# Optimization experiments

Hardware: AMD Instinct MI355X
Metric: run time of the kernel (lower is better)

Reference implementation:

```python
import jax, jax.numpy as jnp
import numpy as np

LOOKBACK = 8
EPS = 1e-6
HID = 32
MV_DIM = 11  # 1 scalar + 4 vector + 6 bivector
# default bivector planes (i, j)
BIV_I = jnp.array([0, 0, 0, 1, 1, 2])
BIV_J = jnp.array([1, 2, 3, 2, 3, 3])


def phi(x):
    # LeakyReLU(x, 0.01) + 1.0
    return jnp.where(x >= 0, x, 0.01 * x) + 1.0


def setup_inputs() -> dict:
    key = jax.random.key(0)
    ks = jax.random.split(key, 10)
    B, L = 8, 16384
    return {
        "x": jax.random.normal(ks[0], (B, L, 4), dtype=jnp.float32),
        "scalar_bias": jax.random.normal(ks[1], (1,), dtype=jnp.float32) * 0.1,
        "vector_scale": 1.0 + jax.random.normal(ks[2], (4,), dtype=jnp.float32) * 0.1,
        "vector_bias": jax.random.normal(ks[3], (4,), dtype=jnp.float32) * 0.1,
        "bivector_weight": 1.0 + jax.random.normal(ks[4], (6,), dtype=jnp.float32) * 0.1,
        "W_Q": jax.random.normal(ks[5], (MV_DIM, HID), dtype=jnp.float32) * 0.3,
        "W_K": jax.random.normal(ks[6], (MV_DIM, HID), dtype=jnp.float32) * 0.3,
        "W_V": jax.random.normal(ks[7], (MV_DIM, HID), dtype=jnp.float32) * 0.3,
        "w_head": jax.random.normal(ks[8], (HID,), dtype=jnp.float32) * 0.18,
        "b_head": jax.random.normal(ks[9], (), dtype=jnp.float32) * 0.1,
    }


def ga_embed(x, scalar_bias, vector_scale, vector_bias, bivector_weight):
    B, L, _ = x.shape
    scalar = jnp.broadcast_to(1.0 + scalar_bias, (B, L, 1))  # [B,L,1]
    vec = x * vector_scale + vector_bias                      # [B,L,4]
    biv = bivector_weight * (x[..., BIV_I] - x[..., BIV_J])   # [B,L,6]
    return jnp.concatenate([scalar, vec, biv], axis=-1)       # [B,L,11]


def reference(x, scalar_bias, vector_scale, vector_bias, bivector_weight,
              W_Q, W_K, W_V, w_head, b_head):
    M = ga_embed(x, scalar_bias, vector_scale, vector_bias, bivector_weight)
    B, L, _ = M.shape
    Q = phi(M @ W_Q)  # [B,L,H]
    K = phi(M @ W_K)
    V = M @ W_V
    T = L - LOOKBACK
    # sliding windows: for output step t (t = LOOKBACK..L-1) window covers [t-Lb, t)
    win_idx = jnp.arange(T)[:, None] + jnp.arange(LOOKBACK)[None, :]  # [T,Lb]
    Kw = K[:, win_idx]  # [B,T,Lb,H]
    Vw = V[:, win_idx]  # [B,T,Lb,H]
    q = Q[:, LOOKBACK:, :]  # [B,T,H]
    # scores_l = q_t . k_l ; num = sum_l scores_l v_l ; den = sum_l scores_l
    # (identical math to q . (sum_l k_l v_l^T) and q . sum_l k_l)
    scores = jnp.einsum('bth,btlh->btl', q, Kw)               # [B,T,Lb]
    num = jnp.einsum('btl,btlg->btg', scores, Vw)             # [B,T,H]
    den = jnp.sum(scores, axis=-1, keepdims=True) + EPS
    contexts = num / den                                      # [B,T,H]
    weights = scores / (jnp.sum(scores, axis=-1, keepdims=True) + EPS)
    predictions = contexts @ w_head + b_head                  # [B,T]
    return predictions, weights
```

## Files before the change

### kernel.cpp

```cpp
#include <hip/hip_runtime.h>

#define LOOKBACK 8
#define HID 32
#define TB 256
#define NPOS (TB + LOOKBACK)
#define KST 36
#define EPS 1e-6f

#define WS_AQ  0
#define WS_CQ  128
#define WS_AK  160
#define WS_CK  288
#define WS_AVW 320
#define WS_CVW 324
#define WS_N   336

__device__ __forceinline__ float phi1(float z) {
    return (z >= 0.0f ? z : 0.01f * z) + 1.0f;
}

__global__ __launch_bounds__(TB) void ga_fused(
    const float* __restrict__ x,
    const float* __restrict__ sbp,
    const float* __restrict__ vsp,
    const float* __restrict__ vbp,
    const float* __restrict__ bwp,
    const float* __restrict__ WQ,
    const float* __restrict__ WK,
    const float* __restrict__ WV,
    const float* __restrict__ wh,
    const float* __restrict__ bhp,
    float* __restrict__ out,
    int B, int L)
{
    const int T   = L - LOOKBACK;
    const int bb  = blockIdx.y;
    const int t0  = blockIdx.x * TB;
    const int tid = threadIdx.x;

    __shared__ float sP[WS_N];
    __shared__ float sK[NPOS * KST];
    __shared__ float sVW[NPOS];

    const int t = t0 + tid;
    const bool valid = (t < T);
    const float4 xq = *reinterpret_cast<const float4*>(
        x + ((size_t)bb * L + (valid ? t + LOOKBACK : 0)) * 4);

    if (tid < 96) {
        const int h   = tid & 31;
        const int mat = tid >> 5;
        const float* W = (mat == 0) ? WQ : (mat == 1) ? WK : WV;
        float w[11];
#pragma unroll
        for (int j = 0; j < 11; ++j) w[j] = W[j * HID + h];

        const float b0 = bwp[0], b1 = bwp[1], b2 = bwp[2];
        const float b3 = bwp[3], b4 = bwp[4], b5 = bwp[5];
        const float v0 = vsp[0], v1 = vsp[1], v2 = vsp[2], v3 = vsp[3];
        const float u0 = vbp[0], u1 = vbp[1], u2 = vbp[2], u3 = vbp[3];
        const float s0 = 1.0f + sbp[0];

        const float a0 = v0*w[1] + b0*w[5] + b1*w[6] + b2*w[7];
        const float a1 = v1*w[2] - b0*w[5] + b3*w[8] + b4*w[9];
        const float a2 = v2*w[3] - b1*w[6] - b3*w[8] + b5*w[10];
        const float a3 = v3*w[4] - b2*w[7] - b4*w[9] - b5*w[10];
        const float c  = s0*w[0] + u0*w[1] + u1*w[2] + u2*w[3] + u3*w[4];

        if (mat == 0) {
            sP[WS_AQ + 0*HID + h] = a0; sP[WS_AQ + 1*HID + h] = a1;
            sP[WS_AQ + 2*HID + h] = a2; sP[WS_AQ + 3*HID + h] = a3;
            sP[WS_CQ + h] = c;
        } else if (mat == 1) {
            sP[WS_AK + 0*HID + h] = a0; sP[WS_AK + 1*HID + h] = a1;
            sP[WS_AK + 2*HID + h] = a2; sP[WS_AK + 3*HID + h] = a3;
            sP[WS_CK + h] = c;
        } else {
            const float ww = wh[h];
            float r[5] = { a0*ww, a1*ww, a2*ww, a3*ww, c*ww };
#pragma unroll
            for (int off = 16; off > 0; off >>= 1) {
#pragma unroll
                for (int i = 0; i < 5; ++i) r[i] += __shfl_down(r[i], off, 32);
            }
            if (h == 0) {
                sP[WS_AVW + 0] = r[0]; sP[WS_AVW + 1] = r[1];
                sP[WS_AVW + 2] = r[2]; sP[WS_AVW + 3] = r[3];
                sP[WS_CVW]     = r[4];
            }
        }
    }
    __syncthreads();

    const float avw0 = sP[WS_AVW + 0], avw1 = sP[WS_AVW + 1];
    const float avw2 = sP[WS_AVW + 2], avw3 = sP[WS_AVW + 3];
    const float cvw  = sP[WS_CVW];

    const int npos = min(NPOS, L - t0);
    for (int pos = tid; pos < npos; pos += TB) {
        const float4 xv = *reinterpret_cast<const float4*>(
            x + ((size_t)bb * L + (t0 + pos)) * 4);

        sVW[pos] = cvw + xv.x*avw0 + xv.y*avw1 + xv.z*avw2 + xv.w*avw3;

#pragma unroll
        for (int g = 0; g < 8; ++g) {
            float4 a = *reinterpret_cast<const float4*>(&sP[WS_CK + g*4]);
#pragma unroll
            for (int d = 0; d < 4; ++d) {
                const float xd = (d == 0) ? xv.x : (d == 1) ? xv.y
                               : (d == 2) ? xv.z : xv.w;
                const float4 ad = *reinterpret_cast<const float4*>(
                    &sP[WS_AK + d*HID + g*4]);
                a.x += xd*ad.x; a.y += xd*ad.y; a.z += xd*ad.z; a.w += xd*ad.w;
            }
            a.x = phi1(a.x); a.y = phi1(a.y); a.z = phi1(a.z); a.w = phi1(a.w);
            *reinterpret_cast<float4*>(&sK[pos * KST + g * 4]) = a;
        }
    }
    __syncthreads();

    if (!valid) return;

    float q[HID];
#pragma unroll
    for (int g = 0; g < 8; ++g) {
        float4 z = *reinterpret_cast<const float4*>(&sP[WS_CQ + g*4]);
#pragma unroll
        for (int d = 0; d < 4; ++d) {
            const float xd = (d == 0) ? xq.x : (d == 1) ? xq.y
                           : (d == 2) ? xq.z : xq.w;
            const float4 ad = *reinterpret_cast<const float4*>(
                &sP[WS_AQ + d*HID + g*4]);
            z.x += xd*ad.x; z.y += xd*ad.y; z.z += xd*ad.z; z.w += xd*ad.w;
        }
        q[g*4+0] = phi1(z.x); q[g*4+1] = phi1(z.y);
        q[g*4+2] = phi1(z.z); q[g*4+3] = phi1(z.w);
    }

    float sc[LOOKBACK];
#pragma unroll
    for (int l = 0; l < LOOKBACK; ++l) sc[l] = 0.0f;

#pragma unroll
    for (int g = 0; g < 8; ++g) {
        const float qx = q[g*4+0], qy = q[g*4+1], qz = q[g*4+2], qw = q[g*4+3];
#pragma unroll
        for (int l = 0; l < LOOKBACK; ++l) {
            const float4 kg = *reinterpret_cast<const float4*>(
                &sK[(tid + l) * KST + g * 4]);
            sc[l] += qx*kg.x + qy*kg.y + qz*kg.z + qw*kg.w;
        }
    }

    float ssum = 0.0f, p = 0.0f;
#pragma unroll
    for (int l = 0; l < LOOKBACK; ++l) {
        ssum += sc[l];
        p    += sc[l] * sVW[tid + l];
    }
    const float inv = 1.0f / (ssum + EPS);

    out[(size_t)bb * T + t] = p * inv + bhp[0];

    float* wout = out + (size_t)B * T + ((size_t)bb * T + t) * LOOKBACK;
    *reinterpret_cast<float4*>(wout) =
        make_float4(sc[0]*inv, sc[1]*inv, sc[2]*inv, sc[3]*inv);
    *reinterpret_cast<float4*>(wout + 4) =
        make_float4(sc[4]*inv, sc[5]*inv, sc[6]*inv, sc[7]*inv);
}

extern "C" void kernel_launch(void* const* d_in, const int* in_sizes, int n_in,
                              void* d_out, int out_size, void* d_ws, size_t ws_size,
                              hipStream_t stream) {
    const float* x  = (const float*)d_in[0];
    const float* sb = (const float*)d_in[1];
    const float* vs = (const float*)d_in[2];
    const float* vb = (const float*)d_in[3];
    const float* bw = (const float*)d_in[4];
    const float* WQ = (const float*)d_in[5];
    const float* WK = (const float*)d_in[6];
    const float* WV = (const float*)d_in[7];
    const float* wh = (const float*)d_in[8];
    const float* bh = (const float*)d_in[9];
    float* out = (float*)d_out;

    const long long bl = (long long)in_sizes[0] / 4;
    const long long bt = (long long)out_size / (1 + LOOKBACK);
    const int B = (int)((bl - bt) / LOOKBACK);
    const int L = (int)(bl / B);
    const int T = L - LOOKBACK;

    dim3 grid((T + TB - 1) / TB, B);
    ga_fused<<<grid, TB, 0, stream>>>(x, sb, vs, vb, bw, WQ, WK, WV, wh, bh,
                                      out, B, L);
}
```

Baseline: 12.75 us.

## Compute two outputs per thread with group-major padded K layout in LDS

Halves the block to 128 threads, and each thread now handles two consecutive time steps, so the 9 K rows it loads serve both outputs' scores. K in shared memory moves from a row-major 36-float stride to a group-major layout with padding every 8 rows, meant to cut LDS bank conflicts on float4 reads. K and VW staging is unrolled to a fixed three rows per thread. The intent is fewer LDS reads per output and fewer block launches, at the cost of more registers per thread and a smaller block.

```diff
diff --git a/kernel.cpp b/kernel.cpp
--- a/kernel.cpp
+++ b/kernel.cpp
@@ -2,9 +2,9 @@
 
 #define LOOKBACK 8
 #define HID 32
-#define TB 256
-#define NPOS (TB + LOOKBACK)
-#define KST 36
+#define TB 128
+#define TPB 256
+#define NR  (TPB + LOOKBACK)
 #define EPS 1e-6f
 
 #define WS_AQ  0
@@ -15,37 +15,44 @@
 #define WS_CVW 324
 #define WS_N   336
 
+#define GSZ 1188
+
 __device__ __forceinline__ float phi1(float z) {
     return (z >= 0.0f ? z : 0.01f * z) + 1.0f;
 }
+__device__ __forceinline__ float dot4(const float4 a, const float4 b) {
+    return a.x*b.x + a.y*b.y + a.z*b.z + a.w*b.w;
+}
 
 __global__ __launch_bounds__(TB) void ga_fused(
     const float* __restrict__ x,
-    const float* __restrict__ sbp,
-    const float* __restrict__ vsp,
-    const float* __restrict__ vbp,
-    const float* __restrict__ bwp,
-    const float* __restrict__ WQ,
-    const float* __restrict__ WK,
-    const float* __restrict__ WV,
-    const float* __restrict__ wh,
+    const float* __restrict__ sbp, const float* __restrict__ vsp,
+    const float* __restrict__ vbp, const float* __restrict__ bwp,
+    const float* __restrict__ WQ,  const float* __restrict__ WK,
+    const float* __restrict__ WV,  const float* __restrict__ wh,
     const float* __restrict__ bhp,
     float* __restrict__ out,
     int B, int L)
 {
     const int T   = L - LOOKBACK;
     const int bb  = blockIdx.y;
-    const int t0  = blockIdx.x * TB;
+    const int t0  = blockIdx.x * TPB;
     const int tid = threadIdx.x;
 
     __shared__ float sP[WS_N];
-    __shared__ float sK[NPOS * KST];
-    __shared__ float sVW[NPOS];
-
-    const int t = t0 + tid;
-    const bool valid = (t < T);
-    const float4 xq = *reinterpret_cast<const float4*>(
-        x + ((size_t)bb * L + (valid ? t + LOOKBACK : 0)) * 4);
+    __shared__ float sK[8 * GSZ];
+    __shared__ float sVW[NR];
+
+    const float* xb = x + (size_t)bb * L * 4;
+
+    const int tl = 2 * tid;
+    const int ta = t0 + tl;
+    const bool va = (ta < T);
+    const bool vb = (ta + 1 < T);
+    const float4 xqa = *reinterpret_cast<const float4*>(
+        xb + (size_t)(va ? ta + LOOKBACK : 0) * 4);
+    const float4 xqb = *reinterpret_cast<const float4*>(
+        xb + (size_t)(vb ? ta + 1 + LOOKBACK : 0) * 4);
 
     if (tid < 96) {
         const int h   = tid & 31;
@@ -92,82 +99,141 @@
     }
     __syncthreads();
 
-    const float avw0 = sP[WS_AVW + 0], avw1 = sP[WS_AVW + 1];
-    const float avw2 = sP[WS_AVW + 2], avw3 = sP[WS_AVW + 3];
-    const float cvw  = sP[WS_CVW];
-
-    const int npos = min(NPOS, L - t0);
-    for (int pos = tid; pos < npos; pos += TB) {
-        const float4 xv = *reinterpret_cast<const float4*>(
-            x + ((size_t)bb * L + (t0 + pos)) * 4);
-
-        sVW[pos] = cvw + xv.x*avw0 + xv.y*avw1 + xv.z*avw2 + xv.w*avw3;
-
-#pragma unroll
-        for (int g = 0; g < 8; ++g) {
-            float4 a = *reinterpret_cast<const float4*>(&sP[WS_CK + g*4]);
-#pragma unroll
-            for (int d = 0; d < 4; ++d) {
-                const float xd = (d == 0) ? xv.x : (d == 1) ? xv.y
-                               : (d == 2) ? xv.z : xv.w;
-                const float4 ad = *reinterpret_cast<const float4*>(
-                    &sP[WS_AK + d*HID + g*4]);
-                a.x += xd*ad.x; a.y += xd*ad.y; a.z += xd*ad.z; a.w += xd*ad.w;
-            }
-            a.x = phi1(a.x); a.y = phi1(a.y); a.z = phi1(a.z); a.w = phi1(a.w);
-            *reinterpret_cast<float4*>(&sK[pos * KST + g * 4]) = a;
+    const int npos = min(NR, L - t0);
+    const int r0 = tid, r1 = tid + TB;
+    const bool has2 = (tid + 2*TB < npos);
+    const int r2 = tid + 2*TB;
+
+    const float4 x0 = *reinterpret_cast<const float4*>(xb + (size_t)(t0 + r0) * 4);
+    const float4 x1 = *reinterpret_cast<const float4*>(xb + (size_t)(t0 + r1) * 4);
+    const float4 x2 = *reinterpret_cast<const float4*>(
+        xb + (size_t)(has2 ? t0 + r2 : t0) * 4);
+
+    {
+        const float avw0 = sP[WS_AVW + 0], avw1 = sP[WS_AVW + 1];
+        const float avw2 = sP[WS_AVW + 2], avw3 = sP[WS_AVW + 3];
+        const float cvw  = sP[WS_CVW];
+        sVW[r0] = cvw + x0.x*avw0 + x0.y*avw1 + x0.z*avw2 + x0.w*avw3;
+        sVW[r1] = cvw + x1.x*avw0 + x1.y*avw1 + x1.z*avw2 + x1.w*avw3;
+        if (has2)
+            sVW[r2] = cvw + x2.x*avw0 + x2.y*avw1 + x2.z*avw2 + x2.w*avw3;
+    }
+
+    const int o0 = r0*4 + (r0>>3)*4;
+    const int o1 = r1*4 + (r1>>3)*4;
+    const int o2 = r2*4 + (r2>>3)*4;
+
+#pragma unroll
+    for (int g = 0; g < 8; ++g) {
+        const float4 c  = *reinterpret_cast<const float4*>(&sP[WS_CK + g*4]);
+        const float4 a0 = *reinterpret_cast<const float4*>(&sP[WS_AK + 0*HID + g*4]);
+        const float4 a1 = *reinterpret_cast<const float4*>(&sP[WS_AK + 1*HID + g*4]);
+        const float4 a2 = *reinterpret_cast<const float4*>(&sP[WS_AK + 2*HID + g*4]);
+        const float4 a3 = *reinterpret_cast<const float4*>(&sP[WS_AK + 3*HID + g*4]);
+
+        float4 k;
+        k.x = c.x + x0.x*a0.x + x0.y*a1.x + x0.z*a2.x + x0.w*a3.x;
+        k.y = c.y + x0.x*a0.y + x0.y*a1.y + x0.z*a2.y + x0.w*a3.y;
+        k.z = c.z + x0.x*a0.z + x0.y*a1.z + x0.z*a2.z + x0.w*a3.z;
+        k.w = c.w + x0.x*a0.w + x0.y*a1.w + x0.z*a2.w + x0.w*a3.w;
+        k.x = phi1(k.x); k.y = phi1(k.y); k.z = phi1(k.z); k.w = phi1(k.w);
+        *reinterpret_cast<float4*>(&sK[g*GSZ + o0]) = k;
+
+        k.x = c.x + x1.x*a0.x + x1.y*a1.x + x1.z*a2.x + x1.w*a3.x;
+        k.y = c.y + x1.x*a0.y + x1.y*a1.y + x1.z*a2.y + x1.w*a3.y;
+        k.z = c.z + x1.x*a0.z + x1.y*a1.z + x1.z*a2.z + x1.w*a3.z;
+        k.w = c.w + x1.x*a0.w + x1.y*a1.w + x1.z*a2.w + x1.w*a3.w;
+        k.x = phi1(k.x); k.y = phi1(k.y); k.z = phi1(k.z); k.w = phi1(k.w);
+        *reinterpret_cast<float4*>(&sK[g*GSZ + o1]) = k;
+
+        if (has2) {
+            k.x = c.x + x2.x*a0.x + x2.y*a1.x + x2.z*a2.x + x2.w*a3.x;
+            k.y = c.y + x2.x*a0.y + x2.y*a1.y + x2.z*a2.y + x2.w*a3.y;
+            k.z = c.z + x2.x*a0.z + x2.y*a1.z + x2.z*a2.z + x2.w*a3.z;
+            k.w = c.w + x2.x*a0.w + x2.y*a1.w + x2.z*a2.w + x2.w*a3.w;
+            k.x = phi1(k.x); k.y = phi1(k.y); k.z = phi1(k.z); k.w = phi1(k.w);
+            *reinterpret_cast<float4*>(&sK[g*GSZ + o2]) = k;
         }
     }
     __syncthreads();
 
-    if (!valid) return;
-
-    float q[HID];
+    if (!va) return;
+
+    float scA[LOOKBACK], scB[LOOKBACK];
+#pragma unroll
+    for (int l = 0; l < LOOKBACK; ++l) { scA[l] = 0.0f; scB[l] = 0.0f; }
+
+    int ro[9];
+#pragma unroll
+    for (int j = 0; j < 9; ++j) {
+        const int r = tl + j;
+        ro[j] = r*4 + (r>>3)*4;
+    }
+
 #pragma unroll
     for (int g = 0; g < 8; ++g) {
-        float4 z = *reinterpret_cast<const float4*>(&sP[WS_CQ + g*4]);
-#pragma unroll
-        for (int d = 0; d < 4; ++d) {
-            const float xd = (d == 0) ? xq.x : (d == 1) ? xq.y
-                           : (d == 2) ? xq.z : xq.w;
-            const float4 ad = *reinterpret_cast<const float4*>(
-                &sP[WS_AQ + d*HID + g*4]);
-            z.x += xd*ad.x; z.y += xd*ad.y; z.z += xd*ad.z; z.w += xd*ad.w;
-        }
-        q[g*4+0] = phi1(z.x); q[g*4+1] = phi1(z.y);
-        q[g*4+2] = phi1(z.z); q[g*4+3] = phi1(z.w);
-    }
-
-    float sc[LOOKBACK];
-#pragma unroll
-    for (int l = 0; l < LOOKBACK; ++l) sc[l] = 0.0f;
-
-#pragma unroll
-    for (int g = 0; g < 8; ++g) {
-        const float qx = q[g*4+0], qy = q[g*4+1], qz = q[g*4+2], qw = q[g*4+3];
-#pragma unroll
-        for (int l = 0; l < LOOKBACK; ++l) {
-            const float4 kg = *reinterpret_cast<const float4*>(
-                &sK[(tid + l) * KST + g * 4]);
-            sc[l] += qx*kg.x + qy*kg.y + qz*kg.z + qw*kg.w;
-        }
-    }
-
-    float ssum = 0.0f, p = 0.0f;
+        const float4 cq = *reinterpret_cast<const float4*>(&sP[WS_CQ + g*4]);
+        const float4 a0 = *reinterpret_cast<const float4*>(&sP[WS_AQ + 0*HID + g*4]);
+        const float4 a1 = *reinterpret_cast<const float4*>(&sP[WS_AQ + 1*HID + g*4]);
+        const float4 a2 = *reinterpret_cast<const float4*>(&sP[WS_AQ + 2*HID + g*4]);
+        const float4 a3 = *reinterpret_cast<const float4*>(&sP[WS_AQ + 3*HID + g*4]);
+
+        float4 qa, qb;
+        qa.x = phi1(cq.x + xqa.x*a0.x + xqa.y*a1.x + xqa.z*a2.x + xqa.w*a3.x);
+        qa.y = phi1(cq.y + xqa.x*a0.y + xqa.y*a1.y + xqa.z*a2.y + xqa.w*a3.y);
+        qa.z = phi1(cq.z + xqa.x*a0.z + xqa.y*a1.z + xqa.z*a2.z + xqa.w*a3.z);
+        qa.w = phi1(cq.w + xqa.x*a0.w + xqa.y*a1.w + xqa.z*a2.w + xqa.w*a3.w);
+        qb.x = phi1(cq.x + xqb.x*a0.x + xqb.y*a1.x + xqb.z*a2.x + xqb.w*a3.x);
+        qb.y = phi1(cq.y + xqb.x*a0.y + xqb.y*a1.y + xqb.z*a2.y + xqb.w*a3.y);
+        qb.z = phi1(cq.z + xqb.x*a0.z + xqb.y*a1.z + xqb.z*a2.z + xqb.w*a3.z);
+        qb.w = phi1(cq.w + xqb.x*a0.w + xqb.y*a1.w + xqb.z*a2.w + xqb.w*a3.w);
+
+        const float* kg = &sK[g * GSZ];
+        float4 k0 = *reinterpret_cast<const float4*>(kg + ro[0]);
+        float4 k1 = *reinterpret_cast<const float4*>(kg + ro[1]);
+        float4 k2 = *reinterpret_cast<const float4*>(kg + ro[2]);
+        float4 k3 = *reinterpret_cast<const float4*>(kg + ro[3]);
+        float4 k4 = *reinterpret_cast<const float4*>(kg + ro[4]);
+        float4 k5 = *reinterpret_cast<const float4*>(kg + ro[5]);
+        float4 k6 = *reinterpret_cast<const float4*>(kg + ro[6]);
+        float4 k7 = *reinterpret_cast<const float4*>(kg + ro[7]);
+        float4 k8 = *reinterpret_cast<const float4*>(kg + ro[8]);
+
+        scA[0] += dot4(qa, k0); scB[0] += dot4(qb, k1);
+        scA[1] += dot4(qa, k1); scB[1] += dot4(qb, k2);
+        scA[2] += dot4(qa, k2); scB[2] += dot4(qb, k3);
+        scA[3] += dot4(qa, k3); scB[3] += dot4(qb, k4);
+        scA[4] += dot4(qa, k4); scB[4] += dot4(qb, k5);
+        scA[5] += dot4(qa, k5); scB[5] += dot4(qb, k6);
+        scA[6] += dot4(qa, k6); scB[6] += dot4(qb, k7);
+        scA[7] += dot4(qa, k7); scB[7] += dot4(qb, k8);
+    }
+
+    const float bh = bhp[0];
+    float ssA = 0.0f, pA = 0.0f, ssB = 0.0f, pB = 0.0f;
 #pragma unroll
     for (int l = 0; l < LOOKBACK; ++l) {
-        ssum += sc[l];
-        p    += sc[l] * sVW[tid + l];
-    }
-    const float inv = 1.0f / (ssum + EPS);
-
-    out[(size_t)bb * T + t] = p * inv + bhp[0];
-
-    float* wout = out + (size_t)B * T + ((size_t)bb * T + t) * LOOKBACK;
-    *reinterpret_cast<float4*>(wout) =
-        make_float4(sc[0]*inv, sc[1]*inv, sc[2]*inv, sc[3]*inv);
-    *reinterpret_cast<float4*>(wout + 4) =
-        make_float4(sc[4]*inv, sc[5]*inv, sc[6]*inv, sc[7]*inv);
+        ssA += scA[l];  pA += scA[l] * sVW[tl + l];
+        ssB += scB[l];  pB += scB[l] * sVW[tl + 1 + l];
+    }
+    const float invA = 1.0f / (ssA + EPS);
+    const float invB = 1.0f / (ssB + EPS);
+
+    out[(size_t)bb * T + ta] = pA * invA + bh;
+    float* wA = out + (size_t)B * T + ((size_t)bb * T + ta) * LOOKBACK;
+    *reinterpret_cast<float4*>(wA) =
+        make_float4(scA[0]*invA, scA[1]*invA, scA[2]*invA, scA[3]*invA);
+    *reinterpret_cast<float4*>(wA + 4) =
+        make_float4(scA[4]*invA, scA[5]*invA, scA[6]*invA, scA[7]*invA);
+
+    if (vb) {
+        out[(size_t)bb * T + ta + 1] = pB * invB + bh;
+        float* wB = wA + LOOKBACK;
+        *reinterpret_cast<float4*>(wB) =
+            make_float4(scB[0]*invB, scB[1]*invB, scB[2]*invB, scB[3]*invB);
+        *reinterpret_cast<float4*>(wB + 4) =
+            make_float4(scB[4]*invB, scB[5]*invB, scB[6]*invB, scB[7]*invB);
+    }
 }
 
 extern "C" void kernel_launch(void* const* d_in, const int* in_sizes, int n_in,
@@ -191,7 +257,7 @@
     const int L = (int)(bl / B);
     const int T = L - LOOKBACK;
 
-    dim3 grid((T + TB - 1) / TB, B);
+    dim3 grid((T + TPB - 1) / TPB, B);
     ga_fused<<<grid, TB, 0, stream>>>(x, sb, vs, vb, bw, WQ, WK, WV, wh, bh,
                                       out, B, L);
 }
```

Result: slower. 14.89 us (+16.7%).
